# Kernel tuning notes

Measured on AMD Instinct MI355X. Metric: run time of the kernel, lower is better.

## Reference

```python
import jax, jax.numpy as jnp
import numpy as np

K = 3            # kernel_size
KK = K * K       # 9 neighbors per pixel
DILATIONS = [1, 2, 3]
NUM_HEADS = 3


def conv2d(x, w, b, dilation, padding):
    # x: [B,Cin,H,W], w: [Cout,Cin,kh,kw]
    out = jax.lax.conv_general_dilated(
        x, w, window_strides=(1, 1),
        padding=((padding, padding), (padding, padding)),
        rhs_dilation=(dilation, dilation),
        dimension_numbers=('NCHW', 'OIHW', 'NCHW'))
    if b is not None:
        out = out + b[None, :, None, None]
    return out


def unfold3(x, dil):
    # nn.Unfold(kernel=3, dilation=dil, padding=dil, stride=1): [B,C,H,W] -> [B, C*9, H*W]
    B, C, H, W = x.shape
    xp = jnp.pad(x, ((0, 0), (0, 0), (dil, dil), (dil, dil)))
    patches = [xp[:, :, i * dil:i * dil + H, j * dil:j * dil + W]
               for i in range(K) for j in range(K)]
    p = jnp.stack(patches, axis=2)          # [B,C,9,H,W] (channel-major like torch unfold)
    return p.reshape(B, C * KK, H * W)


def bilinear_sample(x, py, px):
    # x: [B,C,H,W]; py, px: [B,K2,H,W] float sample coords -> [B,C,K2,H,W]
    B, C, H, W = x.shape
    K2 = py.shape[1]
    y0 = jnp.floor(py); x0 = jnp.floor(px)
    wy = py - y0; wx = px - x0
    x_flat = x.reshape(B, C, H * W)

    def gather(yi, xi):
        yii = yi.astype(jnp.int32); xii = xi.astype(jnp.int32)
        valid = (yii >= 0) & (yii < H) & (xii >= 0) & (xii < W)
        yc = jnp.clip(yii, 0, H - 1); xc = jnp.clip(xii, 0, W - 1)
        idx = (yc * W + xc).reshape(B, -1)                       # [B, K2*H*W]
        vals = jnp.take_along_axis(x_flat, idx[:, None, :], axis=2)
        vals = vals.reshape(B, C, K2, H, W)
        return vals * valid[:, None].astype(x.dtype)

    v00 = gather(y0, x0); v01 = gather(y0, x0 + 1)
    v10 = gather(y0 + 1, x0); v11 = gather(y0 + 1, x0 + 1)
    wy = wy[:, None]; wx = wx[:, None]
    return (v00 * (1 - wy) * (1 - wx) + v01 * (1 - wy) * wx
            + v10 * wy * (1 - wx) + v11 * wy * wx)


def deform_conv(x, offsets, w, b, dil):
    # torchvision DeformConv2d, stride 1, padding=dil, dilation=dil, kernel 3
    B, C, H, W = x.shape
    off = offsets.reshape(B, KK, 2, H, W)                 # [..., (dy,dx), ...]
    ky, kx = jnp.meshgrid(jnp.arange(K), jnp.arange(K), indexing='ij')
    base_dy = (ky.reshape(KK) * dil - dil).astype(x.dtype)
    base_dx = (kx.reshape(KK) * dil - dil).astype(x.dtype)
    hh = jnp.arange(H, dtype=x.dtype); ww = jnp.arange(W, dtype=x.dtype)
    py = hh[None, None, :, None] + base_dy[None, :, None, None] + off[:, :, 0]
    px = ww[None, None, None, :] + base_dx[None, :, None, None] + off[:, :, 1]
    sampled = bilinear_sample(x, py, px)                  # [B,C,9,H,W]
    out = jnp.einsum('bckhw,ock->bohw', sampled, w.reshape(w.shape[0], C, KK))
    return out + b[None, :, None, None]


def adda_attention(q, k, v, head_dim, dil, deform_params):
    # q,k,v: [B,d,H,W] (already stop-gradiented)
    B, d, H, W = q.shape
    scale = head_dim ** -0.5
    if dil != 1:
        ow, ob, dw, db = deform_params
        offsets = conv2d(k, ow, ob, dil, dil)             # [B, 2*9, H, W]
        k = deform_conv(k, offsets, dw, db, dil)
        v = deform_conv(v, offsets, dw, db, dil)
    ku = unfold3(k, dil)                                  # [B, d*9, HW]
    vu = unfold3(v, dil)
    g = d // head_dim
    HW = H * W
    qh = q.reshape(B, g, head_dim, 1, HW).transpose(0, 1, 4, 3, 2)   # [B,g,HW,1,hd]
    kh = ku.reshape(B, g, head_dim, KK, HW).transpose(0, 1, 4, 2, 3) # [B,g,HW,hd,9]
    vh = vu.reshape(B, g, head_dim, KK, HW).transpose(0, 1, 4, 3, 2) # [B,g,HW,9,hd]
    attn = jax.nn.softmax((qh @ kh) * scale, axis=-1)                # [B,g,HW,1,9]
    o = attn @ vh                                                    # [B,g,HW,1,hd]
    return o.transpose(0, 2, 1, 3, 4).reshape(B, H, W, d)


def setup_inputs() -> dict:
    key = jax.random.key(0)
    ks = jax.random.split(key, 16)
    B, H, W, C = 8, 64, 64, 192
    hd = C // NUM_HEADS  # 64 == C // num_dilation
    inp = {
        'x': jax.random.normal(ks[0], (B, H, W, C), jnp.float32),
        'qkv_w': jax.random.normal(ks[1], (3 * C, C, 1, 1), jnp.float32) * 0.05,
        'proj_w': jax.random.normal(ks[2], (C, C), jnp.float32) * 0.05,
        'proj_b': jnp.zeros((C,), jnp.float32),
        'off_w2': jax.random.normal(ks[3], (2 * KK, hd, K, K), jnp.float32) * 0.01,
        'off_b2': jnp.zeros((2 * KK,), jnp.float32),
        'def_w2': jax.random.normal(ks[4], (hd, hd, K, K), jnp.float32) * 0.05,
        'def_b2': jnp.zeros((hd,), jnp.float32),
        'off_w3': jax.random.normal(ks[5], (2 * KK, hd, K, K), jnp.float32) * 0.01,
        'off_b3': jnp.zeros((2 * KK,), jnp.float32),
        'def_w3': jax.random.normal(ks[6], (hd, hd, K, K), jnp.float32) * 0.05,
        'def_b3': jnp.zeros((hd,), jnp.float32),
    }
    return inp


def reference(x, qkv_w, proj_w, proj_b,
              off_w2, off_b2, def_w2, def_b2,
              off_w3, off_b3, def_w3, def_b3):
    B, H, W, C = x.shape
    nd = len(DILATIONS)
    d = C // nd
    hd = C // NUM_HEADS
    xc = x.transpose(0, 3, 1, 2)                              # [B,C,H,W]
    qkv = conv2d(xc, qkv_w, None, 1, 0)                       # [B,3C,H,W]
    qkv = qkv.reshape(B, 3, nd, d, H, W).transpose(2, 1, 0, 3, 4, 5)  # [nd,3,B,d,H,W]
    qkv = jax.lax.stop_gradient(qkv)                          # q,k,v are .detach()'d in torch
    deform = {2: (off_w2, off_b2, def_w2, def_b2),
              3: (off_w3, off_b3, def_w3, def_b3)}
    outs = []
    for i, dil in enumerate(DILATIONS):
        outs.append(adda_attention(qkv[i, 0], qkv[i, 1], qkv[i, 2],
                                   hd, dil, deform.get(dil)))
    out = jnp.stack(outs, axis=3).reshape(B, H, W, C)         # permute(1,2,3,0,4).reshape
    return out @ proj_w.T + proj_b
```

## Files before the change

kernel.cpp:

```cpp
#include <hip/hip_runtime.h>
#include <cmath>

#define kB    8
#define kH    64
#define kW    64
#define kHW   4096
#define kC    192
#define kD    64
#define kM    (kB * kHW)
#define kNQKV 576

typedef unsigned short ushort_t;
typedef __attribute__((ext_vector_type(8))) short  s8v;
typedef __attribute__((ext_vector_type(4))) float  f4v;

__device__ inline unsigned short bf16r(float f) {
    union { float f; unsigned u; } v; v.f = f;
    unsigned u = v.u + 0x7FFFu + ((v.u >> 16) & 1u);
    return (unsigned short)(u >> 16);
}
__device__ inline float bfu(short s) {
    union { unsigned u; float f; } v;
    v.u = ((unsigned)(unsigned short)s) << 16;
    return v.f;
}

__global__ void cvt_prep(const float* __restrict__ x, unsigned* __restrict__ xb,
                         const float* __restrict__ qkv_w,
                         const float* __restrict__ proj_w,
                         const float* __restrict__ def_w2,
                         const float* __restrict__ def_w3,
                         const float* __restrict__ off_w2,
                         const float* __restrict__ off_w3,
                         ushort_t* __restrict__ awb,
                         ushort_t* __restrict__ pwbp,
                         ushort_t* __restrict__ dwtb2,
                         ushort_t* __restrict__ dwtb3,
                         ushort_t* __restrict__ owtb2,
                         ushort_t* __restrict__ owtb3) {
    const int bid = blockIdx.x;
    const int tid = threadIdx.x;
    if (bid < 12288) {
        int i = bid * 256 + tid;
        if (i >= kM * kC / 2) return;
        float2 f = ((const float2*)x)[i];
        xb[i] = (unsigned)bf16r(f.x) | ((unsigned)bf16r(f.y) << 16);
    } else if (bid < 12342) {
        int idx = (bid - 12288) * 256 + tid;
        if (idx >= 36 * 6 * 64) return;
        int lane = idx & 63;
        int kc   = (idx >> 6) % 6;
        int s    = idx / 384;
        int row  = s * 16 + (lane & 15);
        int k0   = kc * 32 + (lane >> 4) * 8;
        const float* src = qkv_w + (size_t)row * kC + k0;
        ushort_t* dst = awb + (size_t)idx * 8;
#pragma unroll
        for (int j = 0; j < 8; ++j) dst[j] = bf16r(src[j]);
    } else if (bid < 12360) {
        int idx = (bid - 12342) * 256 + tid;
        if (idx >= 12 * 6 * 64) return;
        int lane = idx & 63;
        int kc   = (idx >> 6) % 6;
        int s    = idx / 384;
        int row  = s * 16 + (lane & 15);
        int k0   = kc * 32 + (lane >> 4) * 8;
        const float* src = proj_w + (size_t)row * kC + k0;
        ushort_t* dst = pwbp + (size_t)idx * 8;
#pragma unroll
        for (int j = 0; j < 8; ++j) dst[j] = bf16r(src[j]);
    } else if (bid < 12648) {
        const float* dw = (bid < 12504) ? def_w2 : def_w3;
        ushort_t* dwtb  = (bid < 12504) ? dwtb2 : dwtb3;
        int l = ((bid < 12504) ? (bid - 12360) : (bid - 12504)) * 256 + tid;
        if (l >= kD * kD * 9) return;
        int o = l / 576;
        int c = (l / 9) % 64;
        int kk = l % 9;
        dwtb[(kk * 64 + o) * 64 + c] = bf16r(dw[l]);
    } else {
        const float* ow = (bid < 12720) ? off_w2 : off_w3;
        ushort_t* owtb  = (bid < 12720) ? owtb2 : owtb3;
        int l = ((bid < 12720) ? (bid - 12648) : (bid - 12720)) * 256 + tid;
        if (l >= 9 * 32 * 64) return;
        int kk = l >> 11;
        int j  = (l >> 6) & 31;
        int c  = l & 63;
        owtb[l] = (j < 18) ? bf16r(ow[j * 576 + c * 9 + kk]) : (ushort_t)0;
    }
}

__global__ __launch_bounds__(256) void qkv_mfma3(const ushort_t* __restrict__ xb,
                                                 const ushort_t* __restrict__ awb,
                                                 ushort_t* __restrict__ qkvpx) {
    __shared__ ushort_t xs[64 * kC];

    const int tid = threadIdx.x;
    const int bx  = blockIdx.x;
    const int lb  = (bx & 7) * 64 + (bx >> 3);
    const int m0  = lb * 64;
    const int ty3 = blockIdx.y;

#pragma unroll
    for (int i = 0; i < 6; ++i) {
        int il = i * 256 + tid;
        int p  = il / 24;
        int cc = il % 24;
        uint4 v = *(const uint4*)(xb + (size_t)(m0 + p) * kC + cc * 8);
        int dst = p * 384 + ((cc * 16) ^ ((p & 7) << 4));
        *(uint4*)((char*)xs + dst) = v;
    }
    __syncthreads();

    const int lane = tid & 63;
    const int wave = tid >> 6;
    const int l15  = lane & 15;
    const int q    = lane >> 4;
    const int sbase = ty3 * 12 + wave * 3;

    f4v acc[3][4];
#pragma unroll
    for (int i = 0; i < 3; ++i)
#pragma unroll
        for (int m = 0; m < 4; ++m) acc[i][m] = (f4v){0.f, 0.f, 0.f, 0.f};

    const ushort_t* ap = awb + ((size_t)sbase * 6 * 64 + lane) * 8;

#pragma unroll
    for (int kc = 0; kc < 6; ++kc) {
        s8v bfr[4];
#pragma unroll
        for (int m = 0; m < 4; ++m) {
            int row = m * 16 + l15;
            int col = (kc * 64 + q * 16) ^ ((l15 & 7) << 4);
            bfr[m] = *(const s8v*)((const char*)xs + row * 384 + col);
        }
#pragma unroll
        for (int i = 0; i < 3; ++i) {
            s8v a = *(const s8v*)(ap + (size_t)(i * 6 + kc) * 64 * 8);
#pragma unroll
            for (int m = 0; m < 4; ++m)
                acc[i][m] = __builtin_amdgcn_mfma_f32_16x16x32_bf16(a, bfr[m], acc[i][m], 0, 0, 0);
        }
    }

#pragma unroll
    for (int i = 0; i < 3; ++i) {
        int s   = sbase + i;
        int ty  = s >> 2;
        int c64 = (s & 3) * 16 + q * 4;
        ushort_t* obase = qkvpx + (size_t)ty * kM * 64 + (size_t)m0 * 64 + c64;
#pragma unroll
        for (int m = 0; m < 4; ++m) {
            f4v v = acc[i][m];
            uint2 u;
            u.x = (unsigned)bf16r(v.x) | ((unsigned)bf16r(v.y) << 16);
            u.y = (unsigned)bf16r(v.z) | ((unsigned)bf16r(v.w) << 16);
            *(uint2*)(obase + (size_t)(m * 16 + l15) * 64) = u;
        }
    }
}

__global__ __launch_bounds__(256) void off_conv_fused(const ushort_t* __restrict__ k1,
                                                      const ushort_t* __restrict__ k2,
                                                      const ushort_t* __restrict__ owtb2,
                                                      const ushort_t* __restrict__ owtb3,
                                                      const float* __restrict__ ob2,
                                                      const float* __restrict__ ob3,
                                                      float* __restrict__ offb2,
                                                      float* __restrict__ offb3) {
    const int bx = blockIdx.x;
    const int lb = (bx & 7) * 128 + (bx >> 3);
    const int zb = lb >> 9;
    const int rest = lb & 511;
    const int b = rest >> 6;
    const int y = rest & 63;
    const int dil = 2 + zb;
    const ushort_t* kpx  = zb ? k2 : k1;
    const ushort_t* owtb = zb ? owtb3 : owtb2;
    const float* obias   = zb ? ob3 : ob2;
    float* offb          = zb ? offb3 : offb2;

    const int tid  = threadIdx.x;
    const int lane = tid & 63;
    const int wave = tid >> 6;
    const int l15  = lane & 15;
    const int q    = lane >> 4;
    const int px   = wave * 16 + l15;

    const ushort_t* inpx = kpx + (size_t)b * kHW * 64 + q * 8;

    f4v acc[2];
    acc[0] = (f4v){0.f, 0.f, 0.f, 0.f};
    acc[1] = (f4v){0.f, 0.f, 0.f, 0.f};

#pragma unroll
    for (int kk = 0; kk < 9; ++kk) {
        const int yy = y + (kk / 3 - 1) * dil;
        const int xx = px + (kk % 3 - 1) * dil;
        const bool valid = (yy >= 0) & (yy < kH) & (xx >= 0) & (xx < kW);
        const size_t idx = valid ? (size_t)(yy * kW + xx) * 64 : 0;
        s8v a0 = *(const s8v*)(inpx + idx);
        s8v a1 = *(const s8v*)(inpx + idx + 32);
        if (!valid) {
            a0 = (s8v){0, 0, 0, 0, 0, 0, 0, 0};
            a1 = (s8v){0, 0, 0, 0, 0, 0, 0, 0};
        }
        const ushort_t* wb = owtb + (size_t)kk * 2048 + l15 * 64 + q * 8;
#pragma unroll
        for (int nbk = 0; nbk < 2; ++nbk) {
            s8v b0 = *(const s8v*)(wb + nbk * 1024);
            s8v b1 = *(const s8v*)(wb + nbk * 1024 + 32);
            acc[nbk] = __builtin_amdgcn_mfma_f32_16x16x32_bf16(a0, b0, acc[nbk], 0, 0, 0);
            acc[nbk] = __builtin_amdgcn_mfma_f32_16x16x32_bf16(a1, b1, acc[nbk], 0, 0, 0);
        }
    }
#pragma unroll
    for (int nbk = 0; nbk < 2; ++nbk) {
        int n = nbk * 16 + l15;
        if (n < 18) {
            float bias = obias[n];
            f4v v = acc[nbk];
            v.x += bias; v.y += bias; v.z += bias; v.w += bias;
            *(f4v*)&offb[((size_t)b * 18 + n) * kHW + y * kW + wave * 16 + q * 4] = v;
        }
    }
}

__global__ __launch_bounds__(512) void deform_fused(const ushort_t* __restrict__ k1,
                                                    const ushort_t* __restrict__ v1,
                                                    const ushort_t* __restrict__ k2,
                                                    const ushort_t* __restrict__ v2,
                                                    const float* __restrict__ offb2,
                                                    const float* __restrict__ offb3,
                                                    const ushort_t* __restrict__ dwtb2,
                                                    const ushort_t* __restrict__ dwtb3,
                                                    const float* __restrict__ db2,
                                                    const float* __restrict__ db3,
                                                    ushort_t* __restrict__ kd2,
                                                    ushort_t* __restrict__ vd2,
                                                    ushort_t* __restrict__ kd3,
                                                    ushort_t* __restrict__ vd3) {
    __shared__ ushort_t kv[10 * 4096];
    __shared__ ushort_t wlds[9 * 4096];

    const int tid = threadIdx.x;
    const int bx  = blockIdx.x;
    const int lb  = (bx & 7) * 128 + (bx >> 3);
    const int zb  = lb >> 9;
    const int t   = (lb >> 8) & 1;
    const int b   = (lb >> 5) & 7;
    const int y0  = (lb & 31) * 2;
    const int dil = 2 + zb;
    const int nr  = 2 * dil + 4;
    const int wlo = y0 - dil - 1;

    const ushort_t* kin = zb ? k2 : k1;
    const ushort_t* vin = zb ? v2 : v1;
    const float* offbS  = zb ? offb3 : offb2;
    const ushort_t* dwtb = zb ? dwtb3 : dwtb2;
    const float* db      = zb ? db3 : db2;
    ushort_t* outk = zb ? kd3 : kd2;
    ushort_t* outv = zb ? vd3 : vd2;

    const ushort_t* inb = (t ? vin : kin) + (size_t)b * kHW * 64;
    ushort_t* outp = t ? outv : outk;

#pragma unroll
    for (int i = 0; i < 9; ++i) {
        int g = (i * 512 + tid) * 16;
        uint4 v = *(const uint4*)((const char*)dwtb + g);
        int row = (g >> 7) & 63;
        int dst = g ^ ((row & 7) << 4);
        *(uint4*)((char*)wlds + dst) = v;
    }
    {
        int x  = tid >> 3;
        int cc = tid & 7;
        int dstc = (x * 128 + cc * 16) ^ ((x & 7) << 4);
        for (int r = 0; r < nr; ++r) {
            int gy = min(max(wlo + r, 0), kH - 1);
            *(uint4*)((char*)kv + r * 8192 + dstc) =
                *(const uint4*)(inb + (size_t)gy * 4096 + tid * 8);
        }
    }
    __syncthreads();

    const int lane = tid & 63;
    const int wave = tid >> 6;
    const int ry   = wave >> 2;
    const int wc   = wave & 3;
    const int l15  = lane & 15;
    const int q    = lane >> 4;
    const int y    = y0 + ry;
    const int px   = wc * 16 + l15;
    const int wsw  = (l15 & 7) << 4;
    const int wcol0 = (q * 16) ^ wsw;
    const int wcol1 = (q * 16 + 64) ^ wsw;

    const ushort_t* inpx = inb + q * 8;

    f4v acc[4];
#pragma unroll
    for (int ob = 0; ob < 4; ++ob) acc[ob] = (f4v){0.f, 0.f, 0.f, 0.f};

    const float* offrow = offbS + (size_t)b * 18 * kHW + y * kW + px;
    float offv[18];
#pragma unroll
    for (int i = 0; i < 18; ++i) offv[i] = offrow[(size_t)i * kHW];

#pragma unroll
    for (int kk = 0; kk < 9; ++kk) {
        float oy = offv[kk * 2 + 0];
        float ox = offv[kk * 2 + 1];
        float py  = (float)y  + (float)((kk / 3 - 1) * dil) + oy;
        float pxf = (float)px + (float)((kk % 3 - 1) * dil) + ox;
        float fy = floorf(py), fx = floorf(pxf);
        float wy = py - fy, wx = pxf - fx;
        int iy0 = (int)fy, ix0 = (int)fx;
        int iy1 = iy0 + 1, ix1 = ix0 + 1;
        int y0c = min(max(iy0, 0), kH - 1), x0c = min(max(ix0, 0), kW - 1);
        int y1c = min(max(iy1, 0), kH - 1), x1c = min(max(ix1, 0), kW - 1);
        bool vy0 = (iy0 >= 0) & (iy0 < kH), vx0 = (ix0 >= 0) & (ix0 < kW);
        bool vy1 = (iy1 >= 0) & (iy1 < kH), vx1 = (ix1 >= 0) & (ix1 < kW);
        float w0 = (vy0 && vx0) ? (1.f - wy) * (1.f - wx) : 0.f;
        float w1 = (vy0 && vx1) ? (1.f - wy) * wx : 0.f;
        float w2 = (vy1 && vx0) ? wy * (1.f - wx) : 0.f;
        float w3 = (vy1 && vx1) ? wy * wx : 0.f;

        s8v c[8];
        if (__builtin_expect(fabsf(oy) < 1.0f, 1)) {
            int r0 = min(max(y0c - wlo, 0), nr - 1);
            int r1 = min(max(y1c - wlo, 0), nr - 1);
            int b00 = r0 * 8192 + ((x0c * 128 + q * 16) ^ ((x0c & 7) << 4));
            int b00h = r0 * 8192 + ((x0c * 128 + q * 16 + 64) ^ ((x0c & 7) << 4));
            int b01 = r0 * 8192 + ((x1c * 128 + q * 16) ^ ((x1c & 7) << 4));
            int b01h = r0 * 8192 + ((x1c * 128 + q * 16 + 64) ^ ((x1c & 7) << 4));
            int b10 = r1 * 8192 + ((x0c * 128 + q * 16) ^ ((x0c & 7) << 4));
            int b10h = r1 * 8192 + ((x0c * 128 + q * 16 + 64) ^ ((x0c & 7) << 4));
            int b11 = r1 * 8192 + ((x1c * 128 + q * 16) ^ ((x1c & 7) << 4));
            int b11h = r1 * 8192 + ((x1c * 128 + q * 16 + 64) ^ ((x1c & 7) << 4));
            c[0] = *(const s8v*)((const char*)kv + b00);
            c[1] = *(const s8v*)((const char*)kv + b00h);
            c[2] = *(const s8v*)((const char*)kv + b01);
            c[3] = *(const s8v*)((const char*)kv + b01h);
            c[4] = *(const s8v*)((const char*)kv + b10);
            c[5] = *(const s8v*)((const char*)kv + b10h);
            c[6] = *(const s8v*)((const char*)kv + b11);
            c[7] = *(const s8v*)((const char*)kv + b11h);
        } else {
            size_t i00 = (size_t)(y0c * kW + x0c) * 64;
            size_t i01 = (size_t)(y0c * kW + x1c) * 64;
            size_t i10 = (size_t)(y1c * kW + x0c) * 64;
            size_t i11 = (size_t)(y1c * kW + x1c) * 64;
            c[0] = *(const s8v*)(inpx + i00);
            c[1] = *(const s8v*)(inpx + i00 + 32);
            c[2] = *(const s8v*)(inpx + i01);
            c[3] = *(const s8v*)(inpx + i01 + 32);
            c[4] = *(const s8v*)(inpx + i10);
            c[5] = *(const s8v*)(inpx + i10 + 32);
            c[6] = *(const s8v*)(inpx + i11);
            c[7] = *(const s8v*)(inpx + i11 + 32);
        }

        s8v b0, b1;
#pragma unroll
        for (int j = 0; j < 8; ++j) {
            float v0 = w0 * bfu(c[0][j]) + w1 * bfu(c[2][j]) +
                       w2 * bfu(c[4][j]) + w3 * bfu(c[6][j]);
            float v1 = w0 * bfu(c[1][j]) + w1 * bfu(c[3][j]) +
                       w2 * bfu(c[5][j]) + w3 * bfu(c[7][j]);
            b0[j] = (short)bf16r(v0);
            b1[j] = (short)bf16r(v1);
        }
        const char* wkk = (const char*)wlds + kk * 8192 + l15 * 128;
#pragma unroll
        for (int obb = 0; obb < 4; ++obb) {
            s8v a0w = *(const s8v*)(wkk + obb * 2048 + wcol0);
            s8v a1w = *(const s8v*)(wkk + obb * 2048 + wcol1);
            acc[obb] = __builtin_amdgcn_mfma_f32_16x16x32_bf16(a0w, b0, acc[obb], 0, 0, 0);
            acc[obb] = __builtin_amdgcn_mfma_f32_16x16x32_bf16(a1w, b1, acc[obb], 0, 0, 0);
        }
    }

    ushort_t* orow = outp + ((size_t)b * kHW + y * kW + px) * 64 + q * 4;
#pragma unroll
    for (int obb = 0; obb < 4; ++obb) {
        float4 bias = *(const float4*)&db[obb * 16 + q * 4];
        f4v v = acc[obb];
        uint2 u;
        u.x = (unsigned)bf16r(v.x + bias.x) | ((unsigned)bf16r(v.y + bias.y) << 16);
        u.y = (unsigned)bf16r(v.z + bias.z) | ((unsigned)bf16r(v.w + bias.w) << 16);
        *(uint2*)(orow + obb * 16) = u;
    }
}

__global__ __launch_bounds__(512) void attn_fused(const ushort_t* __restrict__ q0,
                                                  const ushort_t* __restrict__ k0,
                                                  const ushort_t* __restrict__ v0,
                                                  const ushort_t* __restrict__ q1,
                                                  const ushort_t* __restrict__ kd2,
                                                  const ushort_t* __restrict__ vd2,
                                                  const ushort_t* __restrict__ q2,
                                                  const ushort_t* __restrict__ kd3,
                                                  const ushort_t* __restrict__ vd3,
                                                  ushort_t* __restrict__ aopx) {
    __shared__ ushort_t ks[8 * 4096];
    __shared__ ushort_t vs[8 * 4096];

    const int tid = threadIdx.x;
    const int bx  = blockIdx.x;
    const int lb  = (bx & 7) * 96 + (bx >> 3);
    const int zb  = lb >> 8;
    const int rest = lb & 255;
    const int b   = rest >> 5;
    const int y0  = (rest & 31) * 2;
    const int dil = zb + 1;
    const int nr  = 2 * dil + 2;
    const int wlo = y0 - dil;

    const ushort_t* qpx = (zb == 0) ? q0 : (zb == 1) ? q1 : q2;
    const ushort_t* kpx = (zb == 0) ? k0 : (zb == 1) ? kd2 : kd3;
    const ushort_t* vpx = (zb == 0) ? v0 : (zb == 1) ? vd2 : vd3;

    const size_t pbase = (size_t)b * kHW;
    const ushort_t* kb = kpx + pbase * 64;
    const ushort_t* vb = vpx + pbase * 64;

    {
        int x  = tid >> 3;
        int cc = tid & 7;
        int dstc = (x * 128 + cc * 16) ^ ((x & 7) << 4);
        for (int r = 0; r < nr; ++r) {
            int gy = min(max(wlo + r, 0), kH - 1);
            *(uint4*)((char*)ks + r * 8192 + dstc) = *(const uint4*)(kb + (size_t)gy * 4096 + tid * 8);
            *(uint4*)((char*)vs + r * 8192 + dstc) = *(const uint4*)(vb + (size_t)gy * 4096 + tid * 8);
        }
    }
    __syncthreads();

    const int wave = tid >> 6;
    const int l    = tid & 63;
    const int ry   = wave >> 2;
    const int wc   = wave & 3;
    const int pxq  = l >> 2;
    const int cg   = l & 3;
    const int y  = y0 + ry;
    const int x_ = wc * 16 + pxq;
    const int p  = y * kW + x_;

    const ushort_t* qb = qpx + (pbase + p) * 64 + cg * 16;
    s8v qv0 = *(const s8v*)qb;
    s8v qv1 = *(const s8v*)(qb + 8);
    float qf[16];
#pragma unroll
    for (int j = 0; j < 8; ++j) { qf[j] = bfu(qv0[j]); qf[8 + j] = bfu(qv1[j]); }

    int a0s[9], a1s[9];
    float msk[9];
#pragma unroll
    for (int kk = 0; kk < 9; ++kk) {
        int dy = (kk / 3 - 1) * dil, dx = (kk % 3 - 1) * dil;
        int yy = y + dy, xx = x_ + dx;
        bool v = (yy >= 0) & (yy < kH) & (xx >= 0) & (xx < kW);
        msk[kk] = v ? 1.f : 0.f;
        int r  = min(max(yy - wlo, 0), nr - 1);
        int xc = min(max(xx, 0), kW - 1);
        int sw = (xc & 7) << 4;
        a0s[kk] = r * 8192 + ((xc * 128 + cg * 32) ^ sw);
        a1s[kk] = r * 8192 + ((xc * 128 + cg * 32 + 16) ^ sw);
    }

    float e[9];
#pragma unroll
    for (int kk = 0; kk < 9; ++kk) {
        s8v k0v = *(const s8v*)((const char*)ks + a0s[kk]);
        s8v k1v = *(const s8v*)((const char*)ks + a1s[kk]);
        float s = 0.f;
#pragma unroll
        for (int j = 0; j < 8; ++j) {
            s += qf[j] * bfu(k0v[j]);
            s += qf[8 + j] * bfu(k1v[j]);
        }
        s += __shfl_xor(s, 1);
        s += __shfl_xor(s, 2);
        e[kk] = s * 0.125f * msk[kk];
    }
    float mx = -1e30f;
#pragma unroll
    for (int kk = 0; kk < 9; ++kk) mx = fmaxf(mx, e[kk]);
    float ssum = 0.f;
#pragma unroll
    for (int kk = 0; kk < 9; ++kk) { e[kk] = __expf(e[kk] - mx); ssum += e[kk]; }
    float inv = 1.f / ssum;
#pragma unroll
    for (int kk = 0; kk < 9; ++kk) e[kk] = e[kk] * inv * msk[kk];

    float acc[16];
#pragma unroll
    for (int j = 0; j < 16; ++j) acc[j] = 0.f;
#pragma unroll
    for (int kk = 0; kk < 9; ++kk) {
        s8v v0v = *(const s8v*)((const char*)vs + a0s[kk]);
        s8v v1v = *(const s8v*)((const char*)vs + a1s[kk]);
        float w = e[kk];
#pragma unroll
        for (int j = 0; j < 8; ++j) {
            acc[j] += w * bfu(v0v[j]);
            acc[8 + j] += w * bfu(v1v[j]);
        }
    }
    unsigned u[8];
#pragma unroll
    for (int i = 0; i < 8; ++i)
        u[i] = (unsigned)bf16r(acc[2 * i]) | ((unsigned)bf16r(acc[2 * i + 1]) << 16);
    ushort_t* ob = aopx + (pbase + p) * kC + zb * 64 + cg * 16;
    *(uint4*)ob = make_uint4(u[0], u[1], u[2], u[3]);
    *(uint4*)(ob + 8) = make_uint4(u[4], u[5], u[6], u[7]);
}

__global__ __launch_bounds__(256) void proj_mfma3(const ushort_t* __restrict__ aopx,
                                                  const ushort_t* __restrict__ pwbp,
                                                  const float* __restrict__ pb,
                                                  float* __restrict__ out) {
    __shared__ ushort_t xs[64 * kC];

    const int tid = threadIdx.x;
    const int bx  = blockIdx.x;
    const int lb  = (bx & 7) * 64 + (bx >> 3);
    const int m0  = lb * 64;

#pragma unroll
    for (int i = 0; i < 6; ++i) {
        int il = i * 256 + tid;
        int p  = il / 24;
        int cc = il % 24;
        uint4 v = *(const uint4*)(aopx + (size_t)(m0 + p) * kC + cc * 8);
        int dst = p * 384 + ((cc * 16) ^ ((p & 7) << 4));
        *(uint4*)((char*)xs + dst) = v;
    }
    __syncthreads();

    const int lane = tid & 63;
    const int wave = tid >> 6;
    const int l15  = lane & 15;
    const int q    = lane >> 4;
    const int sbase = wave * 3;

    f4v acc[3][4];
#pragma unroll
    for (int i = 0; i < 3; ++i)
#pragma unroll
        for (int m = 0; m < 4; ++m) acc[i][m] = (f4v){0.f, 0.f, 0.f, 0.f};

    const ushort_t* ap = pwbp + ((size_t)sbase * 6 * 64 + lane) * 8;

#pragma unroll
    for (int kc = 0; kc < 6; ++kc) {
        s8v bfr[4];
#pragma unroll
        for (int m = 0; m < 4; ++m) {
            int row = m * 16 + l15;
            int col = (kc * 64 + q * 16) ^ ((l15 & 7) << 4);
            bfr[m] = *(const s8v*)((const char*)xs + row * 384 + col);
        }
#pragma unroll
        for (int i = 0; i < 3; ++i) {
            s8v a = *(const s8v*)(ap + (size_t)(i * 6 + kc) * 64 * 8);
#pragma unroll
            for (int m = 0; m < 4; ++m)
                acc[i][m] = __builtin_amdgcn_mfma_f32_16x16x32_bf16(a, bfr[m], acc[i][m], 0, 0, 0);
        }
    }

#pragma unroll
    for (int i = 0; i < 3; ++i) {
        int s  = sbase + i;
        int n0 = s * 16 + q * 4;
        float4 bias = *(const float4*)&pb[n0];
#pragma unroll
        for (int m = 0; m < 4; ++m) {
            f4v v = acc[i][m];
            v.x += bias.x; v.y += bias.y; v.z += bias.z; v.w += bias.w;
            *(f4v*)&out[(size_t)(m0 + m * 16 + l15) * kC + n0] = v;
        }
    }
}

extern "C" void kernel_launch(void* const* d_in, const int* in_sizes, int n_in,
                              void* d_out, int out_size, void* d_ws, size_t ws_size,
                              hipStream_t stream) {
    const float* x      = (const float*)d_in[0];
    const float* qkv_w  = (const float*)d_in[1];
    const float* proj_w = (const float*)d_in[2];
    const float* proj_b = (const float*)d_in[3];
    const float* off_w2 = (const float*)d_in[4];
    const float* off_b2 = (const float*)d_in[5];
    const float* def_w2 = (const float*)d_in[6];
    const float* def_b2 = (const float*)d_in[7];
    const float* off_w3 = (const float*)d_in[8];
    const float* off_b3 = (const float*)d_in[9];
    const float* def_w3 = (const float*)d_in[10];
    const float* def_b3 = (const float*)d_in[11];
    float* out = (float*)d_out;

    float* ws    = (float*)d_ws;
    float* offb2 = ws;
    float* offb3 = offb2 + (size_t)18 * kM;
    ushort_t* us = (ushort_t*)(offb3 + (size_t)18 * kM);
    ushort_t* xb     = us;  us += (size_t)kM * kC;
    ushort_t* qkvpx  = us;  us += (size_t)9 * kM * 64;
    ushort_t* kd2    = us;  us += (size_t)kM * 64;
    ushort_t* vd2    = us;  us += (size_t)kM * 64;
    ushort_t* kd3    = us;  us += (size_t)kM * 64;
    ushort_t* vd3    = us;  us += (size_t)kM * 64;
    ushort_t* aopx   = us;  us += (size_t)kM * kC;
    ushort_t* awb    = us;  us += (size_t)kNQKV * kC;
    ushort_t* pwbp   = us;  us += (size_t)kC * kC;
    ushort_t* dwtb2  = us;  us += kD * kD * 9;
    ushort_t* dwtb3  = us;  us += kD * kD * 9;
    ushort_t* owtb2  = us;  us += 9 * 32 * 64;
    ushort_t* owtb3  = us;  us += 9 * 32 * 64;

    cvt_prep<<<12792, 256, 0, stream>>>(x, (unsigned*)xb, qkv_w, proj_w,
                                        def_w2, def_w3, off_w2, off_w3,
                                        awb, pwbp, dwtb2, dwtb3, owtb2, owtb3);

    ushort_t* q0 = qkvpx;
    ushort_t* q1 = qkvpx + (size_t)1 * kM * 64;
    ushort_t* q2 = qkvpx + (size_t)2 * kM * 64;
    ushort_t* k0 = qkvpx + (size_t)3 * kM * 64;
    ushort_t* k1 = qkvpx + (size_t)4 * kM * 64;
    ushort_t* k2 = qkvpx + (size_t)5 * kM * 64;
    ushort_t* v0 = qkvpx + (size_t)6 * kM * 64;
    ushort_t* v1 = qkvpx + (size_t)7 * kM * 64;
    ushort_t* v2 = qkvpx + (size_t)8 * kM * 64;

    qkv_mfma3<<<dim3(kM / 64, 3), 256, 0, stream>>>(xb, awb, qkvpx);

    off_conv_fused<<<1024, 256, 0, stream>>>(k1, k2, owtb2, owtb3,
                                             off_b2, off_b3, offb2, offb3);

    deform_fused<<<1024, 512, 0, stream>>>(k1, v1, k2, v2, offb2, offb3,
                                           dwtb2, dwtb3, def_b2, def_b3,
                                           kd2, vd2, kd3, vd3);

    attn_fused<<<768, 512, 0, stream>>>(q0, k0, v0, q1, kd2, vd2, q2, kd3, vd3, aopx);

    proj_mfma3<<<512, 256, 0, stream>>>(aopx, pwbp, proj_b, out);
}
```

Before: 219.4 us.

## Double deform block height and stream deform weights in two halves

Result: faster. 209.9 us (-4.3%).

```diff
diff --git a/kernel.cpp b/kernel.cpp
--- a/kernel.cpp
+++ b/kernel.cpp
@@ -227,32 +227,32 @@
     }
 }
 
-__global__ __launch_bounds__(512) void deform_fused(const ushort_t* __restrict__ k1,
-                                                    const ushort_t* __restrict__ v1,
-                                                    const ushort_t* __restrict__ k2,
-                                                    const ushort_t* __restrict__ v2,
-                                                    const float* __restrict__ offb2,
-                                                    const float* __restrict__ offb3,
-                                                    const ushort_t* __restrict__ dwtb2,
-                                                    const ushort_t* __restrict__ dwtb3,
-                                                    const float* __restrict__ db2,
-                                                    const float* __restrict__ db3,
-                                                    ushort_t* __restrict__ kd2,
-                                                    ushort_t* __restrict__ vd2,
-                                                    ushort_t* __restrict__ kd3,
-                                                    ushort_t* __restrict__ vd3) {
-    __shared__ ushort_t kv[10 * 4096];
-    __shared__ ushort_t wlds[9 * 4096];
+__global__ __launch_bounds__(1024) void deform_big(const ushort_t* __restrict__ k1,
+                                                   const ushort_t* __restrict__ v1,
+                                                   const ushort_t* __restrict__ k2,
+                                                   const ushort_t* __restrict__ v2,
+                                                   const float* __restrict__ offb2,
+                                                   const float* __restrict__ offb3,
+                                                   const ushort_t* __restrict__ dwtb2,
+                                                   const ushort_t* __restrict__ dwtb3,
+                                                   const float* __restrict__ db2,
+                                                   const float* __restrict__ db3,
+                                                   ushort_t* __restrict__ kd2,
+                                                   ushort_t* __restrict__ vd2,
+                                                   ushort_t* __restrict__ kd3,
+                                                   ushort_t* __restrict__ vd3) {
+    __shared__ ushort_t kv[12 * 4096];
+    __shared__ ushort_t wlds[5 * 4096];
 
     const int tid = threadIdx.x;
     const int bx  = blockIdx.x;
-    const int lb  = (bx & 7) * 128 + (bx >> 3);
-    const int zb  = lb >> 9;
-    const int t   = (lb >> 8) & 1;
-    const int b   = (lb >> 5) & 7;
-    const int y0  = (lb & 31) * 2;
+    const int lb  = (bx & 7) * 64 + (bx >> 3);
+    const int zb  = lb >> 8;
+    const int t   = (lb >> 7) & 1;
+    const int b   = (lb >> 4) & 7;
+    const int y0  = (lb & 15) * 4;
     const int dil = 2 + zb;
-    const int nr  = 2 * dil + 4;
+    const int nr  = 2 * dil + 6;
     const int wlo = y0 - dil - 1;
 
     const ushort_t* kin = zb ? k2 : k1;
@@ -260,29 +260,30 @@
     const float* offbS  = zb ? offb3 : offb2;
     const ushort_t* dwtb = zb ? dwtb3 : dwtb2;
     const float* db      = zb ? db3 : db2;
-    ushort_t* outk = zb ? kd3 : kd2;
-    ushort_t* outv = zb ? vd3 : vd2;
+    ushort_t* outp = t ? (zb ? vd3 : vd2) : (zb ? kd3 : kd2);
 
     const ushort_t* inb = (t ? vin : kin) + (size_t)b * kHW * 64;
-    ushort_t* outp = t ? outv : outk;
-
-#pragma unroll
-    for (int i = 0; i < 9; ++i) {
-        int g = (i * 512 + tid) * 16;
+
+    {
+        int half  = tid >> 9;
+        int chunk = tid & 511;
+        int xcol  = chunk >> 3;
+        int cc    = chunk & 7;
+        int dstc  = (xcol * 128 + cc * 16) ^ ((xcol & 7) << 4);
+        for (int r0 = 0; r0 < nr; r0 += 2) {
+            int r = r0 + half;
+            if (r < nr) {
+                int gy = min(max(wlo + r, 0), kH - 1);
+                *(uint4*)((char*)kv + r * 8192 + dstc) =
+                    *(const uint4*)(inb + (size_t)gy * 4096 + chunk * 8);
+            }
+        }
+    }
+    for (int i = tid; i < 2560; i += 1024) {
+        int g = i * 16;
         uint4 v = *(const uint4*)((const char*)dwtb + g);
         int row = (g >> 7) & 63;
-        int dst = g ^ ((row & 7) << 4);
-        *(uint4*)((char*)wlds + dst) = v;
-    }
-    {
-        int x  = tid >> 3;
-        int cc = tid & 7;
-        int dstc = (x * 128 + cc * 16) ^ ((x & 7) << 4);
-        for (int r = 0; r < nr; ++r) {
-            int gy = min(max(wlo + r, 0), kH - 1);
-            *(uint4*)((char*)kv + r * 8192 + dstc) =
-                *(const uint4*)(inb + (size_t)gy * 4096 + tid * 8);
-        }
+        *(uint4*)((char*)wlds + (g ^ ((row & 7) << 4))) = v;
     }
     __syncthreads();
 
@@ -309,8 +310,7 @@
 #pragma unroll
     for (int i = 0; i < 18; ++i) offv[i] = offrow[(size_t)i * kHW];
 
-#pragma unroll
-    for (int kk = 0; kk < 9; ++kk) {
+    auto do_tap = [&](int kk, int kkbase) {
         float oy = offv[kk * 2 + 0];
         float ox = offv[kk * 2 + 1];
         float py  = (float)y  + (float)((kk / 3 - 1) * dil) + oy;
@@ -373,7 +373,7 @@
             b0[j] = (short)bf16r(v0);
             b1[j] = (short)bf16r(v1);
         }
-        const char* wkk = (const char*)wlds + kk * 8192 + l15 * 128;
+        const char* wkk = (const char*)wlds + (kk - kkbase) * 8192 + l15 * 128;
 #pragma unroll
         for (int obb = 0; obb < 4; ++obb) {
             s8v a0w = *(const s8v*)(wkk + obb * 2048 + wcol0);
@@ -381,7 +381,20 @@
             acc[obb] = __builtin_amdgcn_mfma_f32_16x16x32_bf16(a0w, b0, acc[obb], 0, 0, 0);
             acc[obb] = __builtin_amdgcn_mfma_f32_16x16x32_bf16(a1w, b1, acc[obb], 0, 0, 0);
         }
-    }
+    };
+
+#pragma unroll
+    for (int kk = 0; kk < 5; ++kk) do_tap(kk, 0);
+    __syncthreads();
+    for (int i = tid; i < 2048; i += 1024) {
+        int g = i * 16;
+        uint4 v = *(const uint4*)((const char*)dwtb + 40960 + g);
+        int row = (g >> 7) & 63;
+        *(uint4*)((char*)wlds + (g ^ ((row & 7) << 4))) = v;
+    }
+    __syncthreads();
+#pragma unroll
+    for (int kk = 5; kk < 9; ++kk) do_tap(kk, 5);
 
     ushort_t* orow = outp + ((size_t)b * kHW + y * kW + px) * 64 + q * 4;
 #pragma unroll
@@ -641,9 +654,9 @@
     off_conv_fused<<<1024, 256, 0, stream>>>(k1, k2, owtb2, owtb3,
                                              off_b2, off_b3, offb2, offb3);
 
-    deform_fused<<<1024, 512, 0, stream>>>(k1, v1, k2, v2, offb2, offb3,
-                                           dwtb2, dwtb3, def_b2, def_b3,
-                                           kd2, vd2, kd3, vd3);
+    deform_big<<<512, 1024, 0, stream>>>(k1, v1, k2, v2, offb2, offb3,
+                                         dwtb2, dwtb3, def_b2, def_b3,
+                                         kd2, vd2, kd3, vd3);
 
     attn_fused<<<768, 512, 0, stream>>>(q0, k0, v0, q1, kd2, vd2, q2, kd3, vd3, aopx);
 
```
